# Performance work log

Measured on AMD Instinct MI355X. Metric: run time of the kernel, lower is better.

## Reference

```python
import jax, jax.numpy as jnp
import numpy as np

NQ = 4            # num_qubits
DIM = 2 ** NQ     # 16-dim complex state

def _rx(theta):
    c = jnp.cos(theta / 2.0); s = jnp.sin(theta / 2.0)
    return jnp.array([[c, -1j * s], [-1j * s, c]], dtype=jnp.complex64)

def _ry(theta):
    c = jnp.cos(theta / 2.0); s = jnp.sin(theta / 2.0)
    return jnp.array([[c, -s], [s, c]], dtype=jnp.complex64)

def _apply_1q(state, q, U):
    # state: [B, 16] complex; apply 2x2 unitary U on qubit q (qubit 0 = MSB)
    B = state.shape[0]
    st = state.reshape((B,) + (2,) * NQ)
    st = jnp.moveaxis(st, 1 + q, -1)
    st = st @ U.T
    st = jnp.moveaxis(st, -1, 1 + q)
    return st.reshape(B, DIM)

def _apply_cnot(state, c, t):
    # flip target qubit t where control qubit c == 1
    B = state.shape[0]
    st = state.reshape((B,) + (2,) * NQ)
    st = jnp.moveaxis(st, (1 + c, 1 + t), (-2, -1))
    st = jnp.stack([st[..., 0, :], st[..., 1, ::-1]], axis=-2)
    st = jnp.moveaxis(st, (-2, -1), (1 + c, 1 + t))
    return st.reshape(B, DIM)

def _circuit(state):
    rx1, ry1 = _rx(0.1), _ry(0.2)
    rx2, ry2 = _rx(0.3), _ry(0.4)
    for q in range(NQ):
        state = _apply_1q(state, q, rx1)
        state = _apply_1q(state, q, ry1)
    for q in range(NQ - 1):
        state = _apply_cnot(state, q, q + 1)
    for q in range(NQ):
        state = _apply_1q(state, q, rx2)
        state = _apply_1q(state, q, ry2)
    return state

def setup_inputs() -> dict:
    key = jax.random.key(0)
    ks = jax.random.split(key, 9)
    B = 65536
    return {
        'x':   jax.random.normal(ks[0], (B, 784), dtype=jnp.float32),
        'We1': jax.random.normal(ks[1], (784, 256), dtype=jnp.float32) * 0.05,
        'be1': jnp.zeros((256,), dtype=jnp.float32),
        'We2': jax.random.normal(ks[2], (256, 32), dtype=jnp.float32) * 0.05,
        'be2': jnp.zeros((32,), dtype=jnp.float32),
        'W1':  jax.random.normal(ks[3], (32, 128), dtype=jnp.float32) * 0.05,
        'b1':  jnp.zeros((128,), dtype=jnp.float32),
        'W2':  jax.random.normal(ks[4], (128, 10), dtype=jnp.float32) * 0.05,
        'b2':  jnp.zeros((10,), dtype=jnp.float32),
    }

def reference(x, We1, be1, We2, be2, W1, b1, W2, b2):
    # encoder: Linear(784,256) -> ReLU -> Linear(256,32) -> Tanh
    h = jax.nn.relu(x @ We1 + be1)
    enc = jnp.tanh(h @ We2 + be2)               # [B, 32]
    psi = (enc[:, :DIM] + 1j * enc[:, DIM:]).astype(jnp.complex64)
    norm = jnp.sqrt(jnp.sum(jnp.abs(psi) ** 2, axis=1, keepdims=True))
    psi = psi / norm
    psi = _circuit(psi)                          # [B, 16] complex
    feat = jnp.concatenate([psi.real, psi.imag], axis=1)  # [B, 32]
    # classifier: Linear(32,128) -> ReLU -> (Dropout=identity in eval) -> Linear(128,10)
    out = jax.nn.relu(feat @ W1 + b1) @ W2 + b2
    return out
```

## Files before the change

kernel.cpp:

```cpp
#include <hip/hip_runtime.h>
#include <stdint.h>

#define DEVINL __device__ __forceinline__

typedef short bf16x8 __attribute__((ext_vector_type(8)));
typedef float f32x4  __attribute__((ext_vector_type(4)));

DEVINL uint16_t f2bf(float f) {
    uint32_t u = __builtin_bit_cast(uint32_t, f);
    uint32_t r = u + 0x7fffu + ((u >> 16) & 1u);
    return (uint16_t)(r >> 16);
}

DEVINL f32x4 mfma16x16x32(bf16x8 a, bf16x8 b, f32x4 c) {
    return __builtin_amdgcn_mfma_f32_16x16x32_bf16(a, b, c, 0, 0, 0);
}

DEVINL void async_load16(const void* g, void* l) {
    __builtin_amdgcn_global_load_lds(
        (const __attribute__((address_space(1))) void*)g,
        (__attribute__((address_space(3))) void*)l, 16, 0, 0);
}

#define WS_WE1T 0
#define WS_H    409600
#define WS_WE2T 33964032
#define WS_W1T  33980416
#define WS_W2T  33988608

__global__ __launch_bounds__(256) void prep_weights(
    const float* __restrict__ We1, const float* __restrict__ We2,
    const float* __restrict__ W1,  const float* __restrict__ W2,
    uint16_t* __restrict__ We1T, uint16_t* __restrict__ We2T,
    uint16_t* __restrict__ W1T,  uint16_t* __restrict__ W2T) {
    int tid = blockIdx.x * 256 + threadIdx.x;
    if (tid < 256 * 800) {
        int n = tid / 800, k = tid % 800;
        We1T[tid] = (k < 784) ? f2bf(We1[k * 256 + n]) : (uint16_t)0;
        return;
    }
    int t2 = tid - 256 * 800;
    if (t2 < 32 * 256) {
        int n = t2 / 256, k = t2 % 256;
        We2T[t2] = f2bf(We2[k * 32 + n]);
        return;
    }
    int t3 = t2 - 32 * 256;
    if (t3 < 128 * 32) {
        int n = t3 / 32, k = t3 % 32;
        W1T[t3] = f2bf(W1[k * 128 + n]);
        return;
    }
    int t4 = t3 - 128 * 32;
    if (t4 < 16 * 128) {
        int n = t4 / 128, k = t4 % 128;
        W2T[t4] = (n < 10) ? f2bf(W2[k * 10 + n]) : (uint16_t)0;
        return;
    }
}

__global__ __launch_bounds__(512, 4) void gemm1_kernel(
    const float* __restrict__ x, const uint16_t* __restrict__ We1T,
    const float* __restrict__ be1, uint16_t* __restrict__ h) {
    __shared__ __align__(16) uint16_t Als[128 * 32];
    __shared__ __align__(16) uint16_t Bls[256 * 32];

    const int t = threadIdx.x;
    const int mbase = blockIdx.x * 128;
    const int w  = t >> 6;
    const int l  = t & 63;
    const int wm = w >> 2;
    const int wn = w & 3;
    const int lm = l & 15;
    const int lq = l >> 4;

    f32x4 acc[4][4] = {};

    const int ar = t >> 2;
    const int aq = t & 3;
    const float* xrow = x + (size_t)(mbase + ar) * 784;

    const int g1 = t, g2 = 512 + t;
    const uint16_t* bp1 = We1T + (size_t)(g1 >> 2) * 800 + (g1 & 3) * 8;
    const uint16_t* bp2 = We1T + (size_t)(g2 >> 2) * 800 + (g2 & 3) * 8;

    float4 va0 = *(const float4*)(xrow + aq * 8);
    float4 va1 = *(const float4*)(xrow + aq * 8 + 4);

    for (int k0 = 0; k0 < 800; k0 += 32) {
        __syncthreads();

        async_load16(bp1 + k0, &Bls[8 * g1]);
        async_load16(bp2 + k0, &Bls[8 * g2]);

        union { uint4 u4; uint16_t us[8]; } pk;
        pk.us[0] = f2bf(va0.x); pk.us[1] = f2bf(va0.y);
        pk.us[2] = f2bf(va0.z); pk.us[3] = f2bf(va0.w);
        pk.us[4] = f2bf(va1.x); pk.us[5] = f2bf(va1.y);
        pk.us[6] = f2bf(va1.z); pk.us[7] = f2bf(va1.w);
        *(uint4*)&Als[8 * t] = pk.u4;

        {
            int kn = k0 + 32;
            if (kn < 800) {
                int c = kn + aq * 8;
                if (c < 784) {
                    va0 = *(const float4*)(xrow + c);
                    va1 = *(const float4*)(xrow + c + 4);
                } else {
                    va0 = make_float4(0.f, 0.f, 0.f, 0.f);
                    va1 = make_float4(0.f, 0.f, 0.f, 0.f);
                }
            }
        }

        __syncthreads();

        bf16x8 afr[4], bfr[4];
        #pragma unroll
        for (int mi = 0; mi < 4; mi++)
            afr[mi] = *(const bf16x8*)&Als[(wm * 64 + mi * 16 + lm) * 32 + lq * 8];
        #pragma unroll
        for (int ni = 0; ni < 4; ni++)
            bfr[ni] = *(const bf16x8*)&Bls[(wn * 64 + ni * 16 + lm) * 32 + lq * 8];
        #pragma unroll
        for (int mi = 0; mi < 4; mi++)
            #pragma unroll
            for (int ni = 0; ni < 4; ni++)
                acc[mi][ni] = mfma16x16x32(afr[mi], bfr[ni], acc[mi][ni]);
    }

    #pragma unroll
    for (int ni = 0; ni < 4; ni++) {
        int n = wn * 64 + ni * 16 + lm;
        float bias = be1[n];
        #pragma unroll
        for (int mi = 0; mi < 4; mi++) {
            #pragma unroll
            for (int i = 0; i < 4; i++) {
                int m = mbase + wm * 64 + mi * 16 + lq * 4 + i;
                float v = acc[mi][ni][i] + bias;
                v = v > 0.f ? v : 0.f;
                h[(size_t)m * 256 + n] = f2bf(v);
            }
        }
    }
}

DEVINL void apply_rx(float* sr, float* si, int bit, float c, float s) {
    #pragma unroll
    for (int i = 0; i < 16; i++) {
        if (!(i & bit)) {
            int j = i | bit;
            float r0 = sr[i], i0 = si[i], r1 = sr[j], i1 = si[j];
            sr[i] = c * r0 + s * i1;  si[i] = c * i0 - s * r1;
            sr[j] = c * r1 + s * i0;  si[j] = c * i1 - s * r0;
        }
    }
}
DEVINL void apply_ry(float* sr, float* si, int bit, float c, float s) {
    #pragma unroll
    for (int i = 0; i < 16; i++) {
        if (!(i & bit)) {
            int j = i | bit;
            float r0 = sr[i], i0 = si[i], r1 = sr[j], i1 = si[j];
            sr[i] = c * r0 - s * r1;  si[i] = c * i0 - s * i1;
            sr[j] = s * r0 + c * r1;  si[j] = s * i0 + c * i1;
        }
    }
}
DEVINL void apply_cnot(float* sr, float* si, int cb, int tb) {
    #pragma unroll
    for (int i = 0; i < 16; i++) {
        if ((i & cb) && !(i & tb)) {
            int j = i | tb;
            float tr = sr[i]; sr[i] = sr[j]; sr[j] = tr;
            float ti = si[i]; si[i] = si[j]; si[j] = ti;
        }
    }
}
DEVINL void circuit(float* sr, float* si) {
    const float C1 = 0.99875026039496628f, S1 = 0.04997916927067833f;
    const float C2 = 0.99500416527802582f, S2 = 0.09983341664682815f;
    const float C3 = 0.98877107793604227f, S3 = 0.14943813247359922f;
    const float C4 = 0.98006657784124163f, S4 = 0.19866933079506122f;
    #pragma unroll
    for (int q = 0; q < 4; q++) {
        int bit = 8 >> q;
        apply_rx(sr, si, bit, C1, S1);
        apply_ry(sr, si, bit, C2, S2);
    }
    apply_cnot(sr, si, 8, 4);
    apply_cnot(sr, si, 4, 2);
    apply_cnot(sr, si, 2, 1);
    #pragma unroll
    for (int q = 0; q < 4; q++) {
        int bit = 8 >> q;
        apply_rx(sr, si, bit, C3, S3);
        apply_ry(sr, si, bit, C4, S4);
    }
}

__global__ __launch_bounds__(256) void tail_kernel(
    const uint16_t* __restrict__ h, const uint16_t* __restrict__ We2T,
    const float* __restrict__ be2,
    const uint16_t* __restrict__ W1T, const float* __restrict__ b1,
    const uint16_t* __restrict__ W2T, const float* __restrict__ b2,
    float* __restrict__ out) {
    __shared__ __align__(16) uint16_t hls[64 * 264];
    __shared__ __align__(16) uint16_t we2ls[32 * 264];
    __shared__ __align__(16) uint16_t w1ls[128 * 40];
    __shared__ __align__(16) uint16_t w2ls[16 * 136];

    const int t = threadIdx.x;
    const int rowbase = blockIdx.x * 64;
    const int w  = t >> 6;
    const int l  = t & 63;
    const int lm = l & 15;
    const int lq = l >> 4;

    #pragma unroll
    for (int v = 0; v < 8; v++) {
        int c = t * 8 + v;
        int r = c >> 5, c8 = (c & 31) * 8;
        *(uint4*)&hls[r * 264 + c8] = *(const uint4*)&h[(size_t)(rowbase + r) * 256 + c8];
    }
    #pragma unroll
    for (int v = 0; v < 4; v++) {
        int c = t * 4 + v;
        int r = c >> 5, c8 = (c & 31) * 8;
        *(uint4*)&we2ls[r * 264 + c8] = *(const uint4*)&We2T[r * 256 + c8];
    }
    #pragma unroll
    for (int v = 0; v < 2; v++) {
        int c = t * 2 + v;
        int r = c >> 2, c8 = (c & 3) * 8;
        *(uint4*)&w1ls[r * 40 + c8] = *(const uint4*)&W1T[r * 32 + c8];
    }
    {
        int r = t >> 4, c8 = (t & 15) * 8;
        *(uint4*)&w2ls[r * 136 + c8] = *(const uint4*)&W2T[r * 128 + c8];
    }
    __syncthreads();

    f32x4 acc2[2] = {};
    #pragma unroll
    for (int k0 = 0; k0 < 256; k0 += 32) {
        bf16x8 af = *(const bf16x8*)&hls[(w * 16 + lm) * 264 + k0 + lq * 8];
        #pragma unroll
        for (int ni = 0; ni < 2; ni++) {
            bf16x8 bf = *(const bf16x8*)&we2ls[(ni * 16 + lm) * 264 + k0 + lq * 8];
            acc2[ni] = mfma16x16x32(af, bf, acc2[ni]);
        }
    }
    __syncthreads();

    float* encls = (float*)hls;
    uint16_t* featls = ((uint16_t*)hls) + 4224;
    uint16_t* a1ls   = ((uint16_t*)hls) + 6784;

    #pragma unroll
    for (int ni = 0; ni < 2; ni++) {
        int col = ni * 16 + lm;
        float bias = be2[col];
        #pragma unroll
        for (int i = 0; i < 4; i++) {
            int r = w * 16 + lq * 4 + i;
            encls[r * 33 + col] = tanhf(acc2[ni][i] + bias);
        }
    }
    __syncthreads();

    if (t < 64) {
        float e[32];
        #pragma unroll
        for (int j = 0; j < 32; j++) e[j] = encls[t * 33 + j];
        float s = 0.f;
        #pragma unroll
        for (int j = 0; j < 32; j++) s += e[j] * e[j];
        float inv = 1.0f / sqrtf(s);
        float sr[16], si[16];
        #pragma unroll
        for (int i = 0; i < 16; i++) { sr[i] = e[i] * inv; si[i] = e[16 + i] * inv; }
        circuit(sr, si);
        #pragma unroll
        for (int i = 0; i < 16; i++) {
            featls[t * 40 + i]      = f2bf(sr[i]);
            featls[t * 40 + 16 + i] = f2bf(si[i]);
        }
    }
    __syncthreads();

    f32x4 acc3[8] = {};
    {
        bf16x8 af = *(const bf16x8*)&featls[(w * 16 + lm) * 40 + lq * 8];
        #pragma unroll
        for (int ni = 0; ni < 8; ni++) {
            bf16x8 bf = *(const bf16x8*)&w1ls[(ni * 16 + lm) * 40 + lq * 8];
            acc3[ni] = mfma16x16x32(af, bf, acc3[ni]);
        }
    }
    #pragma unroll
    for (int ni = 0; ni < 8; ni++) {
        int col = ni * 16 + lm;
        float bias = b1[col];
        #pragma unroll
        for (int i = 0; i < 4; i++) {
            int r = w * 16 + lq * 4 + i;
            float v = acc3[ni][i] + bias;
            v = v > 0.f ? v : 0.f;
            a1ls[r * 136 + col] = f2bf(v);
        }
    }
    __syncthreads();

    f32x4 acc4 = {};
    #pragma unroll
    for (int k0 = 0; k0 < 128; k0 += 32) {
        bf16x8 af = *(const bf16x8*)&a1ls[(w * 16 + lm) * 136 + k0 + lq * 8];
        bf16x8 bf = *(const bf16x8*)&w2ls[lm * 136 + k0 + lq * 8];
        acc4 = mfma16x16x32(af, bf, acc4);
    }
    if (lm < 10) {
        float bias = b2[lm];
        #pragma unroll
        for (int i = 0; i < 4; i++) {
            int r = rowbase + w * 16 + lq * 4 + i;
            out[(size_t)r * 10 + lm] = acc4[i] + bias;
        }
    }
}

extern "C" void kernel_launch(void* const* d_in, const int* in_sizes, int n_in,
                              void* d_out, int out_size, void* d_ws, size_t ws_size,
                              hipStream_t stream) {
    const float* x   = (const float*)d_in[0];
    const float* We1 = (const float*)d_in[1];
    const float* be1 = (const float*)d_in[2];
    const float* We2 = (const float*)d_in[3];
    const float* be2 = (const float*)d_in[4];
    const float* W1  = (const float*)d_in[5];
    const float* b1  = (const float*)d_in[6];
    const float* W2  = (const float*)d_in[7];
    const float* b2  = (const float*)d_in[8];
    float* out = (float*)d_out;

    char* ws = (char*)d_ws;
    uint16_t* We1T = (uint16_t*)(ws + WS_WE1T);
    uint16_t* hbuf = (uint16_t*)(ws + WS_H);
    uint16_t* We2T = (uint16_t*)(ws + WS_WE2T);
    uint16_t* W1T  = (uint16_t*)(ws + WS_W1T);
    uint16_t* W2T  = (uint16_t*)(ws + WS_W2T);

    hipLaunchKernelGGL(prep_weights, dim3(856), dim3(256), 0, stream,
                       We1, We2, W1, W2, We1T, We2T, W1T, W2T);
    hipLaunchKernelGGL(gemm1_kernel, dim3(512), dim3(512), 0, stream,
                       x, We1T, be1, hbuf);
    hipLaunchKernelGGL(tail_kernel, dim3(1024), dim3(256), 0, stream,
                       hbuf, We2T, be2, W1T, b1, W2T, b2, out);
}
```

Baseline: 333.2 us.

## Fuse encoder GEMM1 with tail stages to keep hidden tile in LDS

Merges the first encoder GEMM and the tail kernel into one kernel with 64-row tiles. The 256-wide hidden activation stays in shared memory, so the bf16 round trip of h through global memory and one kernel launch go away. Small weight matrices are now read straight from global (L2/cache) instead of staged into LDS. In exchange, the GEMM1 M-tile shrinks from 128 to 64 rows, so every block loads the full We1 K-slice for half as many rows, which doubles weight traffic and lowers MFMA reuse.

New measurement: 343.4 us. +3.1%, slower.

```diff
diff --git a/kernel.cpp b/kernel.cpp
--- a/kernel.cpp
+++ b/kernel.cpp
@@ -23,10 +23,9 @@
 }
 
 #define WS_WE1T 0
-#define WS_H    409600
-#define WS_WE2T 33964032
-#define WS_W1T  33980416
-#define WS_W2T  33988608
+#define WS_WE2T 409600
+#define WS_W1T  425984
+#define WS_W2T  434176
 
 __global__ __launch_bounds__(256) void prep_weights(
     const float* __restrict__ We1, const float* __restrict__ We2,
@@ -59,18 +58,78 @@
     }
 }
 
-__global__ __launch_bounds__(512, 4) void gemm1_kernel(
+DEVINL void apply_rx(float* sr, float* si, int bit, float c, float s) {
+    #pragma unroll
+    for (int i = 0; i < 16; i++) {
+        if (!(i & bit)) {
+            int j = i | bit;
+            float r0 = sr[i], i0 = si[i], r1 = sr[j], i1 = si[j];
+            sr[i] = c * r0 + s * i1;  si[i] = c * i0 - s * r1;
+            sr[j] = c * r1 + s * i0;  si[j] = c * i1 - s * r0;
+        }
+    }
+}
+DEVINL void apply_ry(float* sr, float* si, int bit, float c, float s) {
+    #pragma unroll
+    for (int i = 0; i < 16; i++) {
+        if (!(i & bit)) {
+            int j = i | bit;
+            float r0 = sr[i], i0 = si[i], r1 = sr[j], i1 = si[j];
+            sr[i] = c * r0 - s * r1;  si[i] = c * i0 - s * i1;
+            sr[j] = s * r0 + c * r1;  si[j] = s * i0 + c * i1;
+        }
+    }
+}
+DEVINL void apply_cnot(float* sr, float* si, int cb, int tb) {
+    #pragma unroll
+    for (int i = 0; i < 16; i++) {
+        if ((i & cb) && !(i & tb)) {
+            int j = i | tb;
+            float tr = sr[i]; sr[i] = sr[j]; sr[j] = tr;
+            float ti = si[i]; si[i] = si[j]; si[j] = ti;
+        }
+    }
+}
+DEVINL void circuit(float* sr, float* si) {
+    const float C1 = 0.99875026039496628f, S1 = 0.04997916927067833f;
+    const float C2 = 0.99500416527802582f, S2 = 0.09983341664682815f;
+    const float C3 = 0.98877107793604227f, S3 = 0.14943813247359922f;
+    const float C4 = 0.98006657784124163f, S4 = 0.19866933079506122f;
+    #pragma unroll
+    for (int q = 0; q < 4; q++) {
+        int bit = 8 >> q;
+        apply_rx(sr, si, bit, C1, S1);
+        apply_ry(sr, si, bit, C2, S2);
+    }
+    apply_cnot(sr, si, 8, 4);
+    apply_cnot(sr, si, 4, 2);
+    apply_cnot(sr, si, 2, 1);
+    #pragma unroll
+    for (int q = 0; q < 4; q++) {
+        int bit = 8 >> q;
+        apply_rx(sr, si, bit, C3, S3);
+        apply_ry(sr, si, bit, C4, S4);
+    }
+}
+
+__global__ __launch_bounds__(256, 2) void fused_kernel(
     const float* __restrict__ x, const uint16_t* __restrict__ We1T,
-    const float* __restrict__ be1, uint16_t* __restrict__ h) {
-    __shared__ __align__(16) uint16_t Als[128 * 32];
-    __shared__ __align__(16) uint16_t Bls[256 * 32];
+    const float* __restrict__ be1,
+    const uint16_t* __restrict__ We2T, const float* __restrict__ be2,
+    const uint16_t* __restrict__ W1T, const float* __restrict__ b1,
+    const uint16_t* __restrict__ W2T, const float* __restrict__ b2,
+    float* __restrict__ out) {
+    __shared__ __align__(16) char smem[55296];
+    uint16_t* Htile  = (uint16_t*)smem;
+    uint16_t* Als    = (uint16_t*)(smem + 34816);
+    uint16_t* Bls    = (uint16_t*)(smem + 38912);
+    float*    encls  = (float*)(smem + 34816);
+    uint16_t* featls = (uint16_t*)(smem + 43264);
 
     const int t = threadIdx.x;
-    const int mbase = blockIdx.x * 128;
+    const int rowbase = blockIdx.x * 64;
     const int w  = t >> 6;
     const int l  = t & 63;
-    const int wm = w >> 2;
-    const int wn = w & 3;
     const int lm = l & 15;
     const int lq = l >> 4;
 
@@ -78,11 +137,7 @@
 
     const int ar = t >> 2;
     const int aq = t & 3;
-    const float* xrow = x + (size_t)(mbase + ar) * 784;
-
-    const int g1 = t, g2 = 512 + t;
-    const uint16_t* bp1 = We1T + (size_t)(g1 >> 2) * 800 + (g1 & 3) * 8;
-    const uint16_t* bp2 = We1T + (size_t)(g2 >> 2) * 800 + (g2 & 3) * 8;
+    const float* xrow = x + (size_t)(rowbase + ar) * 784;
 
     float4 va0 = *(const float4*)(xrow + aq * 8);
     float4 va1 = *(const float4*)(xrow + aq * 8 + 4);
@@ -90,16 +145,17 @@
     for (int k0 = 0; k0 < 800; k0 += 32) {
         __syncthreads();
 
-        async_load16(bp1 + k0, &Bls[8 * g1]);
-        async_load16(bp2 + k0, &Bls[8 * g2]);
-
+        #pragma unroll
+        for (int j = 0; j < 4; j++) {
+            int g = j * 256 + t;
+            async_load16(We1T + (size_t)(g >> 2) * 800 + (g & 3) * 8 + k0, &Bls[8 * g]);
+        }
         union { uint4 u4; uint16_t us[8]; } pk;
         pk.us[0] = f2bf(va0.x); pk.us[1] = f2bf(va0.y);
         pk.us[2] = f2bf(va0.z); pk.us[3] = f2bf(va0.w);
         pk.us[4] = f2bf(va1.x); pk.us[5] = f2bf(va1.y);
         pk.us[6] = f2bf(va1.z); pk.us[7] = f2bf(va1.w);
         *(uint4*)&Als[8 * t] = pk.u4;
-
         {
             int kn = k0 + 32;
             if (kn < 800) {
@@ -113,16 +169,15 @@
                 }
             }
         }
-
         __syncthreads();
 
         bf16x8 afr[4], bfr[4];
         #pragma unroll
         for (int mi = 0; mi < 4; mi++)
-            afr[mi] = *(const bf16x8*)&Als[(wm * 64 + mi * 16 + lm) * 32 + lq * 8];
+            afr[mi] = *(const bf16x8*)&Als[(mi * 16 + lm) * 32 + lq * 8];
         #pragma unroll
         for (int ni = 0; ni < 4; ni++)
-            bfr[ni] = *(const bf16x8*)&Bls[(wn * 64 + ni * 16 + lm) * 32 + lq * 8];
+            bfr[ni] = *(const bf16x8*)&Bls[(w * 64 + ni * 16 + lm) * 32 + lq * 8];
         #pragma unroll
         for (int mi = 0; mi < 4; mi++)
             #pragma unroll
@@ -132,133 +187,31 @@
 
     #pragma unroll
     for (int ni = 0; ni < 4; ni++) {
-        int n = wn * 64 + ni * 16 + lm;
+        int n = w * 64 + ni * 16 + lm;
         float bias = be1[n];
         #pragma unroll
         for (int mi = 0; mi < 4; mi++) {
             #pragma unroll
             for (int i = 0; i < 4; i++) {
-                int m = mbase + wm * 64 + mi * 16 + lq * 4 + i;
+                int r = mi * 16 + lq * 4 + i;
                 float v = acc[mi][ni][i] + bias;
                 v = v > 0.f ? v : 0.f;
-                h[(size_t)m * 256 + n] = f2bf(v);
+                Htile[r * 272 + n] = f2bf(v);
             }
         }
     }
-}
-
-DEVINL void apply_rx(float* sr, float* si, int bit, float c, float s) {
-    #pragma unroll
-    for (int i = 0; i < 16; i++) {
-        if (!(i & bit)) {
-            int j = i | bit;
-            float r0 = sr[i], i0 = si[i], r1 = sr[j], i1 = si[j];
-            sr[i] = c * r0 + s * i1;  si[i] = c * i0 - s * r1;
-            sr[j] = c * r1 + s * i0;  si[j] = c * i1 - s * r0;
-        }
-    }
-}
-DEVINL void apply_ry(float* sr, float* si, int bit, float c, float s) {
-    #pragma unroll
-    for (int i = 0; i < 16; i++) {
-        if (!(i & bit)) {
-            int j = i | bit;
-            float r0 = sr[i], i0 = si[i], r1 = sr[j], i1 = si[j];
-            sr[i] = c * r0 - s * r1;  si[i] = c * i0 - s * i1;
-            sr[j] = s * r0 + c * r1;  si[j] = s * i0 + c * i1;
-        }
-    }
-}
-DEVINL void apply_cnot(float* sr, float* si, int cb, int tb) {
-    #pragma unroll
-    for (int i = 0; i < 16; i++) {
-        if ((i & cb) && !(i & tb)) {
-            int j = i | tb;
-            float tr = sr[i]; sr[i] = sr[j]; sr[j] = tr;
-            float ti = si[i]; si[i] = si[j]; si[j] = ti;
-        }
-    }
-}
-DEVINL void circuit(float* sr, float* si) {
-    const float C1 = 0.99875026039496628f, S1 = 0.04997916927067833f;
-    const float C2 = 0.99500416527802582f, S2 = 0.09983341664682815f;
-    const float C3 = 0.98877107793604227f, S3 = 0.14943813247359922f;
-    const float C4 = 0.98006657784124163f, S4 = 0.19866933079506122f;
-    #pragma unroll
-    for (int q = 0; q < 4; q++) {
-        int bit = 8 >> q;
-        apply_rx(sr, si, bit, C1, S1);
-        apply_ry(sr, si, bit, C2, S2);
-    }
-    apply_cnot(sr, si, 8, 4);
-    apply_cnot(sr, si, 4, 2);
-    apply_cnot(sr, si, 2, 1);
-    #pragma unroll
-    for (int q = 0; q < 4; q++) {
-        int bit = 8 >> q;
-        apply_rx(sr, si, bit, C3, S3);
-        apply_ry(sr, si, bit, C4, S4);
-    }
-}
-
-__global__ __launch_bounds__(256) void tail_kernel(
-    const uint16_t* __restrict__ h, const uint16_t* __restrict__ We2T,
-    const float* __restrict__ be2,
-    const uint16_t* __restrict__ W1T, const float* __restrict__ b1,
-    const uint16_t* __restrict__ W2T, const float* __restrict__ b2,
-    float* __restrict__ out) {
-    __shared__ __align__(16) uint16_t hls[64 * 264];
-    __shared__ __align__(16) uint16_t we2ls[32 * 264];
-    __shared__ __align__(16) uint16_t w1ls[128 * 40];
-    __shared__ __align__(16) uint16_t w2ls[16 * 136];
-
-    const int t = threadIdx.x;
-    const int rowbase = blockIdx.x * 64;
-    const int w  = t >> 6;
-    const int l  = t & 63;
-    const int lm = l & 15;
-    const int lq = l >> 4;
-
-    #pragma unroll
-    for (int v = 0; v < 8; v++) {
-        int c = t * 8 + v;
-        int r = c >> 5, c8 = (c & 31) * 8;
-        *(uint4*)&hls[r * 264 + c8] = *(const uint4*)&h[(size_t)(rowbase + r) * 256 + c8];
-    }
-    #pragma unroll
-    for (int v = 0; v < 4; v++) {
-        int c = t * 4 + v;
-        int r = c >> 5, c8 = (c & 31) * 8;
-        *(uint4*)&we2ls[r * 264 + c8] = *(const uint4*)&We2T[r * 256 + c8];
-    }
-    #pragma unroll
-    for (int v = 0; v < 2; v++) {
-        int c = t * 2 + v;
-        int r = c >> 2, c8 = (c & 3) * 8;
-        *(uint4*)&w1ls[r * 40 + c8] = *(const uint4*)&W1T[r * 32 + c8];
-    }
-    {
-        int r = t >> 4, c8 = (t & 15) * 8;
-        *(uint4*)&w2ls[r * 136 + c8] = *(const uint4*)&W2T[r * 128 + c8];
-    }
     __syncthreads();
 
     f32x4 acc2[2] = {};
     #pragma unroll
     for (int k0 = 0; k0 < 256; k0 += 32) {
-        bf16x8 af = *(const bf16x8*)&hls[(w * 16 + lm) * 264 + k0 + lq * 8];
+        bf16x8 af = *(const bf16x8*)&Htile[(w * 16 + lm) * 272 + k0 + lq * 8];
         #pragma unroll
         for (int ni = 0; ni < 2; ni++) {
-            bf16x8 bf = *(const bf16x8*)&we2ls[(ni * 16 + lm) * 264 + k0 + lq * 8];
+            bf16x8 bf = *(const bf16x8*)&We2T[(ni * 16 + lm) * 256 + k0 + lq * 8];
             acc2[ni] = mfma16x16x32(af, bf, acc2[ni]);
         }
     }
-    __syncthreads();
-
-    float* encls = (float*)hls;
-    uint16_t* featls = ((uint16_t*)hls) + 4224;
-    uint16_t* a1ls   = ((uint16_t*)hls) + 6784;
-
     #pragma unroll
     for (int ni = 0; ni < 2; ni++) {
         int col = ni * 16 + lm;
@@ -291,12 +244,13 @@
     }
     __syncthreads();
 
+    uint16_t* a1ls = (uint16_t*)smem;
     f32x4 acc3[8] = {};
     {
         bf16x8 af = *(const bf16x8*)&featls[(w * 16 + lm) * 40 + lq * 8];
         #pragma unroll
         for (int ni = 0; ni < 8; ni++) {
-            bf16x8 bf = *(const bf16x8*)&w1ls[(ni * 16 + lm) * 40 + lq * 8];
+            bf16x8 bf = *(const bf16x8*)&W1T[(ni * 16 + lm) * 32 + lq * 8];
             acc3[ni] = mfma16x16x32(af, bf, acc3[ni]);
         }
     }
@@ -312,13 +266,12 @@
             a1ls[r * 136 + col] = f2bf(v);
         }
     }
-    __syncthreads();
 
     f32x4 acc4 = {};
     #pragma unroll
     for (int k0 = 0; k0 < 128; k0 += 32) {
         bf16x8 af = *(const bf16x8*)&a1ls[(w * 16 + lm) * 136 + k0 + lq * 8];
-        bf16x8 bf = *(const bf16x8*)&w2ls[lm * 136 + k0 + lq * 8];
+        bf16x8 bf = *(const bf16x8*)&W2T[lm * 128 + k0 + lq * 8];
         acc4 = mfma16x16x32(af, bf, acc4);
     }
     if (lm < 10) {
@@ -347,15 +300,12 @@
 
     char* ws = (char*)d_ws;
     uint16_t* We1T = (uint16_t*)(ws + WS_WE1T);
-    uint16_t* hbuf = (uint16_t*)(ws + WS_H);
     uint16_t* We2T = (uint16_t*)(ws + WS_WE2T);
     uint16_t* W1T  = (uint16_t*)(ws + WS_W1T);
     uint16_t* W2T  = (uint16_t*)(ws + WS_W2T);
 
     hipLaunchKernelGGL(prep_weights, dim3(856), dim3(256), 0, stream,
                        We1, We2, W1, W2, We1T, We2T, W1T, W2T);
-    hipLaunchKernelGGL(gemm1_kernel, dim3(512), dim3(512), 0, stream,
-                       x, We1T, be1, hbuf);
-    hipLaunchKernelGGL(tail_kernel, dim3(1024), dim3(256), 0, stream,
-                       hbuf, We2T, be2, W1T, b1, W2T, b2, out);
-}
+    hipLaunchKernelGGL(fused_kernel, dim3(1024), dim3(256), 0, stream,
+                       x, We1T, be1, We2T, be2, W1T, b1, W2T, b2, out);
+}
```
